# Kernel optimization log

Hardware: AMD Instinct MI355X
Metric: run time of the kernel (lower is better)

## Reference

```python
import jax, jax.numpy as jnp
import numpy as np

N_NODES = 10000
N_EDGES = 160000
N_GRAPHS = 64
IN_DIM, HID, HEADS, OUT_DIM = 128, 64, 8, 10
NEG_SLOPE = 0.2


def setup_inputs() -> dict:
    key = jax.random.key(0)
    ks = jax.random.split(key, 20)
    x = jax.random.normal(ks[0], (N_NODES, IN_DIM), dtype=jnp.float32)
    edge_index = jax.random.randint(ks[1], (2, N_EDGES), 0, N_NODES, dtype=jnp.int64)
    batch = jnp.sort(jax.random.randint(ks[2], (N_NODES,), 0, N_GRAPHS, dtype=jnp.int64))

    def glorot(k, shape):
        fan_in, fan_out = shape[0], shape[-1]
        lim = jnp.sqrt(6.0 / (fan_in + fan_out)).astype(jnp.float32)
        return jax.random.uniform(k, shape, jnp.float32, -lim, lim)

    d0 = HID * HEADS  # 512
    params = {
        # layer 0: IN_DIM -> HID x HEADS, concat
        'W0': glorot(ks[3], (IN_DIM, HEADS * HID)),
        'asrc0': glorot(ks[4], (HEADS, HID)), 'adst0': glorot(ks[5], (HEADS, HID)),
        'b0': jnp.zeros((HEADS * HID,), jnp.float32),
        # layer 1: 512 -> HID x HEADS, concat
        'W1': glorot(ks[6], (d0, HEADS * HID)),
        'asrc1': glorot(ks[7], (HEADS, HID)), 'adst1': glorot(ks[8], (HEADS, HID)),
        'b1': jnp.zeros((HEADS * HID,), jnp.float32),
        # layer 2: 512 -> HID, heads=1
        'W2': glorot(ks[9], (d0, HID)),
        'asrc2': glorot(ks[10], (1, HID)), 'adst2': glorot(ks[11], (1, HID)),
        'b2': jnp.zeros((HID,), jnp.float32),
        # classifier: 2*HID -> HID -> OUT_DIM
        'cW1': glorot(ks[12], (2 * HID, HID)), 'cb1': jnp.zeros((HID,), jnp.float32),
        'cW2': glorot(ks[13], (HID, OUT_DIM)), 'cb2': jnp.zeros((OUT_DIM,), jnp.float32),
    }
    return {'x': x, 'edge_index': edge_index, 'batch': batch, **params}


def gat_conv(h_in, src, dst, W, a_src, a_dst, b, heads, ch):
    # PyG GATConv (concat=True, negative_slope=0.2), dropout inactive (eval).
    N = h_in.shape[0]
    h = (h_in @ W).reshape(N, heads, ch)                       # [N,H,C]
    a_s = jnp.sum(h * a_src[None], axis=-1)                    # [N,H]
    a_d = jnp.sum(h * a_dst[None], axis=-1)                    # [N,H]
    e = jax.nn.leaky_relu(a_s[src] + a_d[dst], NEG_SLOPE)      # [E,H]
    # per-destination segment softmax (stable)
    m = jax.ops.segment_max(e, dst, num_segments=N)            # [N,H]
    ex = jnp.exp(e - m[dst])
    s = jax.ops.segment_sum(ex, dst, num_segments=N)
    alpha = ex / (s[dst] + 1e-16)                              # [E,H]
    out = jax.ops.segment_sum(h[src] * alpha[:, :, None], dst, num_segments=N)
    return out.reshape(N, heads * ch) + b


def _forward(x, src, dst, batch,
             W0, asrc0, adst0, b0, W1, asrc1, adst1, b1,
             W2, asrc2, adst2, b2, cW1, cb1, cW2, cb2):
    h = gat_conv(x, src, dst, W0, asrc0, adst0, b0, HEADS, HID)
    h = jax.nn.relu(h)
    h = gat_conv(h, src, dst, W1, asrc1, adst1, b1, HEADS, HID)
    h = jax.nn.relu(h)
    h = gat_conv(h, src, dst, W2, asrc2, adst2, b2, 1, HID)    # [N,HID]
    # global mean + max pool over graphs
    sums = jax.ops.segment_sum(h, batch, num_segments=N_GRAPHS)
    cnt = jax.ops.segment_sum(jnp.ones((h.shape[0], 1), h.dtype), batch, num_segments=N_GRAPHS)
    mean = sums / jnp.maximum(cnt, 1.0)
    mx = jax.ops.segment_max(h, batch, num_segments=N_GRAPHS)
    g = jnp.concatenate([mean, mx], axis=1)                    # [G, 2*HID]
    g = jax.nn.relu(g @ cW1 + cb1)
    return g @ cW2 + cb2                                       # [G, OUT_DIM]


def reference(x, edge_index, batch,
              W0, asrc0, adst0, b0, W1, asrc1, adst1, b1,
              W2, asrc2, adst2, b2, cW1, cb1, cW2, cb2):
    # PyG GATConv adds self-loops by default
    loops = jnp.arange(x.shape[0], dtype=edge_index.dtype)
    src = jnp.concatenate([edge_index[0], loops])
    dst = jnp.concatenate([edge_index[1], loops])
    return _forward(x, src, dst, batch,
                    W0, asrc0, adst0, b0, W1, asrc1, adst1, b1,
                    W2, asrc2, adst2, b2, cW1, cb1, cW2, cb2)
```

## Files before the change

kernel.cpp:

```cpp
#include <hip/hip_runtime.h>
#include <hip/hip_bf16.h>
#include <math.h>

#define NN 10000
#define EIN 160000
#define ETOT 170000
#define NG 64
#define INDIM 128
#define HID 64
#define HEADS 8
#define D0 512
#define OUTD 10

using bfrag = __attribute__((ext_vector_type(8))) short;
using ffrag = __attribute__((ext_vector_type(4))) float;

__device__ inline float bf2f(unsigned short u) { return __uint_as_float(((unsigned)u) << 16); }
__device__ inline unsigned short f2bf(float f) {
    __hip_bfloat16 b = __float2bfloat16(f);
    return *reinterpret_cast<unsigned short*>(&b);
}

__device__ void transpose_tile(const float* __restrict__ src, __hip_bfloat16* __restrict__ dst,
                               int R, int C, int bx, int by) {
    __shared__ float tile[32][33];
    int cb = bx * 32, rb = by * 32;
    int tx = threadIdx.x & 31, ty = threadIdx.x >> 5;
#pragma unroll
    for (int i = 0; i < 32; i += 8) {
        int r = rb + ty + i, c = cb + tx;
        tile[ty + i][tx] = (r < R && c < C) ? src[(size_t)r * C + c] : 0.f;
    }
    __syncthreads();
#pragma unroll
    for (int i = 0; i < 32; i += 8) {
        int c = cb + ty + i, r = rb + tx;
        if (c < C && r < R) dst[(size_t)c * R + r] = __float2bfloat16(tile[tx][ty + i]);
    }
}

__global__ __launch_bounds__(256) void prep_kernel(const float* __restrict__ x,
                                                   const float* __restrict__ W0,
                                                   const float* __restrict__ W1,
                                                   const float* __restrict__ W2,
                                                   __hip_bfloat16* __restrict__ xb,
                                                   __hip_bfloat16* __restrict__ W0T,
                                                   __hip_bfloat16* __restrict__ W1T,
                                                   __hip_bfloat16* __restrict__ W2T,
                                                   int* __restrict__ cnt) {
    int bid = blockIdx.x;
    if (bid < 5000) {
        int i = bid * 256 + threadIdx.x;
        xb[i] = __float2bfloat16(x[i]);
    } else if (bid < 5064) {
        int lb = bid - 5000;
        transpose_tile(W0, W0T, INDIM, D0, lb & 15, lb >> 4);
    } else if (bid < 5320) {
        int lb = bid - 5064;
        transpose_tile(W1, W1T, D0, D0, lb & 15, lb >> 4);
    } else if (bid < 5352) {
        int lb = bid - 5320;
        transpose_tile(W2, W2T, D0, 64, lb & 1, lb >> 1);
    } else {
        int i = (bid - 5352) * 256 + threadIdx.x;
        if (i < NN) cnt[i] = 0;
    }
}

__global__ void count_kernel(const int* __restrict__ ei, int* __restrict__ cnt) {
    int i = blockIdx.x * 256 + threadIdx.x;
    if (i >= ETOT) return;
    int dst = (i < EIN) ? ei[EIN + i] : (i - EIN);
    atomicAdd(&cnt[dst], 1);
}

__global__ __launch_bounds__(1024) void scan_kernel(const int* __restrict__ cnt,
                                                    int* __restrict__ row_ptr,
                                                    int* __restrict__ cursor) {
    __shared__ int ssum[1024];
    int t = threadIdx.x;
    const int PER = 10;
    int base = t * PER;
    int loc[PER];
    int s = 0;
#pragma unroll
    for (int i = 0; i < PER; i++) {
        int v = (base + i < NN) ? cnt[base + i] : 0;
        loc[i] = s; s += v;
    }
    ssum[t] = s;
    __syncthreads();
    for (int off = 1; off < 1024; off <<= 1) {
        int v = (t >= off) ? ssum[t - off] : 0;
        __syncthreads();
        ssum[t] += v;
        __syncthreads();
    }
    int bs = (t > 0) ? ssum[t - 1] : 0;
#pragma unroll
    for (int i = 0; i < PER; i++) {
        if (base + i < NN) { int v = bs + loc[i]; row_ptr[base + i] = v; cursor[base + i] = v; }
    }
    if (t == 0) row_ptr[NN] = ssum[1023];
}

__global__ void scatter_kernel(const int* __restrict__ ei, int* __restrict__ cursor,
                               int* __restrict__ col_src) {
    int i = blockIdx.x * 256 + threadIdx.x;
    if (i >= ETOT) return;
    int src, dst;
    if (i < EIN) { src = ei[i]; dst = ei[EIN + i]; }
    else { src = i - EIN; dst = src; }
    int pos = atomicAdd(&cursor[dst], 1);
    col_src[pos] = src;
}

#define GBM 128
#define GBN 128
#define GBK 32
#define LPAD 8

__global__ __launch_bounds__(256) void gemm_attn(const __hip_bfloat16* __restrict__ A,
                                                 const __hip_bfloat16* __restrict__ BT,
                                                 float* __restrict__ C,
                                                 __hip_bfloat16* __restrict__ Cb,
                                                 const float* __restrict__ asrc,
                                                 const float* __restrict__ adst,
                                                 float* __restrict__ a_s,
                                                 float* __restrict__ a_d,
                                                 int H, int M, int N, int K) {
    __shared__ __align__(16) short As[GBM][GBK + LPAD];
    __shared__ __align__(16) short Bs[GBN][GBK + LPAD];
    int tid = threadIdx.x;
    int wid = tid >> 6, lane = tid & 63;
    int wr = wid >> 1, wc = wid & 1;
    int brow = blockIdx.y * GBM, bcol = blockIdx.x * GBN;

    ffrag acc[4][4] = {};

    int srow = tid >> 2;
    int skq  = (tid & 3) * 8;

    int kq = (lane >> 4) * 8;
    int ra = lane & 15;

    for (int k0 = 0; k0 < K; k0 += GBK) {
#pragma unroll
        for (int p = 0; p < 2; ++p) {
            int r = srow + p * 64;
            int gr = brow + r;
            bfrag va = {0,0,0,0,0,0,0,0};
            if (gr < M) va = *(const bfrag*)(A + (size_t)gr * K + k0 + skq);
            *(bfrag*)&As[r][skq] = va;
            int gc = bcol + r;
            bfrag vb = {0,0,0,0,0,0,0,0};
            if (gc < N) vb = *(const bfrag*)(BT + (size_t)gc * K + k0 + skq);
            *(bfrag*)&Bs[r][skq] = vb;
        }
        __syncthreads();
        bfrag af[4], bf[4];
#pragma unroll
        for (int m = 0; m < 4; ++m) af[m] = *(const bfrag*)&As[wr * 64 + m * 16 + ra][kq];
#pragma unroll
        for (int n = 0; n < 4; ++n) bf[n] = *(const bfrag*)&Bs[wc * 64 + n * 16 + ra][kq];
#pragma unroll
        for (int m = 0; m < 4; ++m)
#pragma unroll
            for (int n = 0; n < 4; ++n)
                acc[m][n] = __builtin_amdgcn_mfma_f32_16x16x32_bf16(af[m], bf[n], acc[m][n], 0, 0, 0);
        __syncthreads();
    }

    int cr = (lane >> 4) * 4;
    int cc = lane & 15;

#pragma unroll
    for (int m = 0; m < 4; ++m) {
#pragma unroll
        for (int n = 0; n < 4; ++n) {
#pragma unroll
            for (int r = 0; r < 4; ++r) {
                int grow = brow + wr * 64 + m * 16 + cr + r;
                int gcol = bcol + wc * 64 + n * 16 + cc;
                if (grow < M && gcol < N) {
                    float v = acc[m][n][r];
                    if (C)  C[(size_t)grow * N + gcol] = v;
                    if (Cb) Cb[(size_t)grow * N + gcol] = __float2bfloat16(v);
                }
            }
        }
    }

    int head = (bcol >> 6) + wc;
    if (head < H) {
        float asl[4], adl[4];
        int cbase = head * 64;
#pragma unroll
        for (int n = 0; n < 4; ++n) {
            asl[n] = asrc[cbase + n * 16 + cc];
            adl[n] = adst[cbase + n * 16 + cc];
        }
#pragma unroll
        for (int m = 0; m < 4; ++m) {
#pragma unroll
            for (int r = 0; r < 4; ++r) {
                float ps = 0.f, pd = 0.f;
#pragma unroll
                for (int n = 0; n < 4; ++n) {
                    float av = acc[m][n][r];
                    ps += av * asl[n];
                    pd += av * adl[n];
                }
#pragma unroll
                for (int o = 1; o < 16; o <<= 1) {
                    ps += __shfl_xor(ps, o);
                    pd += __shfl_xor(pd, o);
                }
                if (cc == 0) {
                    int row = brow + wr * 64 + m * 16 + cr + r;
                    if (row < M) {
                        a_s[(size_t)row * H + head] = ps;
                        a_d[(size_t)row * H + head] = pd;
                    }
                }
            }
        }
    }
}

__global__ __launch_bounds__(256) void gat_agg8(const __hip_bfloat16* __restrict__ h,
                                                const float* __restrict__ a_s,
                                                const float* __restrict__ a_d,
                                                const int* __restrict__ row_ptr,
                                                const int* __restrict__ col_src,
                                                const float* __restrict__ bias,
                                                __hip_bfloat16* __restrict__ out)
{
    int n = blockIdx.x;
    int tid = threadIdx.x;
    int hh = tid >> 5;
    int c0 = tid * 2;
    int r0 = row_ptr[n], r1 = row_ptr[n + 1];

    __shared__ float ad_sh[8];
    __shared__ float al_sh[32][8];
    __shared__ int   src_sh[32];
    if (tid < 8) ad_sh[tid] = a_d[n * 8 + tid];

    float acc0 = 0.f, acc1 = 0.f, ss = 0.f;
    const unsigned short* hu = (const unsigned short*)h;

    for (int kb = r0; kb < r1; kb += 32) {
        __syncthreads();
        {
            int eb = tid >> 3, h8 = tid & 7;
            int k = kb + eb;
            int kc = (k < r1) ? k : r1 - 1;
            int s = col_src[kc];
            if (h8 == 0) src_sh[eb] = s;
            float e = a_s[s * 8 + h8] + ad_sh[h8];
            e = e > 0.f ? e : 0.2f * e;
            float al = __expf(e);
            al_sh[eb][h8] = (k < r1) ? al : 0.f;
        }
        __syncthreads();
        int nb = (r1 - kb < 32) ? (r1 - kb) : 32;
        for (int j = 0; j < nb; j += 8) {
            int s[8]; float al[8]; unsigned v[8];
#pragma unroll
            for (int i = 0; i < 8; ++i) s[i] = src_sh[j + i];
#pragma unroll
            for (int i = 0; i < 8; ++i) al[i] = al_sh[j + i][hh];
#pragma unroll
            for (int i = 0; i < 8; ++i) v[i] = *(const unsigned*)(hu + (size_t)s[i] * 512 + c0);
#pragma unroll
            for (int i = 0; i < 8; ++i) {
                acc0 += al[i] * bf2f((unsigned short)(v[i] & 0xffff));
                acc1 += al[i] * bf2f((unsigned short)(v[i] >> 16));
                ss += al[i];
            }
        }
    }
    float inv = 1.f / (ss + 1e-16f);
    float2 bv = *(const float2*)(bias + c0);
    float o0 = fmaxf(acc0 * inv + bv.x, 0.f);
    float o1 = fmaxf(acc1 * inv + bv.y, 0.f);
    unsigned pk = (unsigned)f2bf(o0) | ((unsigned)f2bf(o1) << 16);
    *(unsigned*)((unsigned short*)out + (size_t)n * 512 + c0) = pk;
}

__global__ __launch_bounds__(256) void gat_agg1(const float* __restrict__ h,
                                                const float* __restrict__ a_s,
                                                const float* __restrict__ a_d,
                                                const int* __restrict__ row_ptr,
                                                const int* __restrict__ col_src,
                                                const float* __restrict__ bias,
                                                float* __restrict__ out) {
    int n = blockIdx.x * 4 + (threadIdx.x >> 6);
    int lane = threadIdx.x & 63;
    if (n >= NN) return;
    int r0 = row_ptr[n], r1 = row_ptr[n + 1];
    float ad = a_d[n];
    float acc = 0.f, ssum = 0.f;
    for (int k = r0; k < r1; k += 8) {
        int kk[8]; int s[8]; float av[8]; float v[8];
#pragma unroll
        for (int i = 0; i < 8; ++i) kk[i] = (k + i < r1) ? k + i : r1 - 1;
#pragma unroll
        for (int i = 0; i < 8; ++i) s[i] = col_src[kk[i]];
#pragma unroll
        for (int i = 0; i < 8; ++i) av[i] = a_s[s[i]];
#pragma unroll
        for (int i = 0; i < 8; ++i) v[i] = h[(size_t)s[i] * 64 + lane];
#pragma unroll
        for (int i = 0; i < 8; ++i) {
            float e = av[i] + ad;
            e = e > 0.f ? e : 0.2f * e;
            float al = __expf(e);
            al = (k + i < r1) ? al : 0.f;
            acc += al * v[i];
            ssum += al;
        }
    }
    out[(size_t)n * 64 + lane] = acc / (ssum + 1e-16f) + bias[lane];
}

__global__ __launch_bounds__(256) void pool_classify(const float* __restrict__ h,
                                                     const int* __restrict__ batch,
                                                     const float* __restrict__ cW1, const float* __restrict__ cb1,
                                                     const float* __restrict__ cW2, const float* __restrict__ cb2,
                                                     float* __restrict__ out) {
    int g = blockIdx.x;
    int tid = threadIdx.x;
    int lane = tid & 63, w = tid >> 6;

    int lo = 0, hi = NN;
    while (lo < hi) { int mid = (lo + hi) >> 1; if (batch[mid] < g) lo = mid + 1; else hi = mid; }
    int s = lo;
    lo = s; hi = NN;
    while (lo < hi) { int mid = (lo + hi) >> 1; if (batch[mid] < g + 1) lo = mid + 1; else hi = mid; }
    int e = lo;

    float sum = 0.f, mx = -1e30f;
    for (int n = s + w; n < e; n += 4) {
        float v = h[(size_t)n * 64 + lane];
        sum += v; mx = fmaxf(mx, v);
    }
    __shared__ float ssum[4][64], smax[4][64];
    __shared__ float gv[128], c1[64];
    ssum[w][lane] = sum; smax[w][lane] = mx;
    __syncthreads();
    if (tid < 64) {
        float s4 = ssum[0][tid] + ssum[1][tid] + ssum[2][tid] + ssum[3][tid];
        float m4 = fmaxf(fmaxf(smax[0][tid], smax[1][tid]), fmaxf(smax[2][tid], smax[3][tid]));
        int cntv = e - s;
        float c = (float)(cntv > 1 ? cntv : 1);
        gv[tid] = s4 / c;
        gv[64 + tid] = m4;
    }
    __syncthreads();
    if (tid < 64) {
        float acc = cb1[tid];
        for (int k = 0; k < 128; k++) acc += gv[k] * cW1[k * 64 + tid];
        c1[tid] = fmaxf(acc, 0.f);
    }
    __syncthreads();
    if (tid < OUTD) {
        float o = cb2[tid];
        for (int k = 0; k < 64; k++) o += c1[k] * cW2[k * OUTD + tid];
        out[g * OUTD + tid] = o;
    }
}

extern "C" void kernel_launch(void* const* d_in, const int* in_sizes, int n_in,
                              void* d_out, int out_size, void* d_ws, size_t ws_size,
                              hipStream_t stream) {
    const float* x     = (const float*)d_in[0];
    const int*   ei    = (const int*)d_in[1];
    const int*   batch = (const int*)d_in[2];
    const float* W0    = (const float*)d_in[3];
    const float* asrc0 = (const float*)d_in[4];
    const float* adst0 = (const float*)d_in[5];
    const float* b0    = (const float*)d_in[6];
    const float* W1    = (const float*)d_in[7];
    const float* asrc1 = (const float*)d_in[8];
    const float* adst1 = (const float*)d_in[9];
    const float* b1    = (const float*)d_in[10];
    const float* W2    = (const float*)d_in[11];
    const float* asrc2 = (const float*)d_in[12];
    const float* adst2 = (const float*)d_in[13];
    const float* b2    = (const float*)d_in[14];
    const float* cW1   = (const float*)d_in[15];
    const float* cb1   = (const float*)d_in[16];
    const float* cW2   = (const float*)d_in[17];
    const float* cb2   = (const float*)d_in[18];
    float* out = (float*)d_out;

    char* ws = (char*)d_ws;
    size_t off = 0;
    auto alloc = [&](size_t bytes) { void* p = ws + off; off += (bytes + 255) & ~(size_t)255; return p; };
    __hip_bfloat16* bufAb = (__hip_bfloat16*)alloc((size_t)NN * D0 * 2);
    __hip_bfloat16* bufBb = (__hip_bfloat16*)alloc((size_t)NN * D0 * 2);
    float* bufC  = (float*)alloc((size_t)NN * 64 * 4);
    float* bufD  = (float*)alloc((size_t)NN * 64 * 4);
    __hip_bfloat16* xb   = (__hip_bfloat16*)alloc((size_t)NN * INDIM * 2);
    __hip_bfloat16* W0T  = (__hip_bfloat16*)alloc((size_t)D0 * INDIM * 2);
    __hip_bfloat16* W1T  = (__hip_bfloat16*)alloc((size_t)D0 * D0 * 2);
    __hip_bfloat16* W2T  = (__hip_bfloat16*)alloc((size_t)64 * D0 * 2);
    float* a_s     = (float*)alloc((size_t)NN * HEADS * 4);
    float* a_d     = (float*)alloc((size_t)NN * HEADS * 4);
    int*   cnt     = (int*)alloc((size_t)NN * 4);
    int*   row_ptr = (int*)alloc((size_t)(NN + 1) * 4);
    int*   cursor  = (int*)alloc((size_t)NN * 4);
    int*   col_src = (int*)alloc((size_t)(ETOT + 8) * 4);
    (void)ws_size; (void)n_in; (void)in_sizes; (void)out_size;

    prep_kernel<<<5392, 256, 0, stream>>>(x, W0, W1, W2, xb, W0T, W1T, W2T, cnt);

    count_kernel<<<(ETOT + 255) / 256, 256, 0, stream>>>(ei, cnt);
    scan_kernel<<<1, 1024, 0, stream>>>(cnt, row_ptr, cursor);
    scatter_kernel<<<(ETOT + 255) / 256, 256, 0, stream>>>(ei, cursor, col_src);

    dim3 gg8(D0 / GBN, (NN + GBM - 1) / GBM);
    dim3 gg1(1, (NN + GBM - 1) / GBM);

    gemm_attn<<<gg8, 256, 0, stream>>>(xb, W0T, nullptr, bufAb, asrc0, adst0, a_s, a_d, HEADS, NN, D0, INDIM);
    gat_agg8<<<NN, 256, 0, stream>>>(bufAb, a_s, a_d, row_ptr, col_src, b0, bufBb);

    gemm_attn<<<gg8, 256, 0, stream>>>(bufBb, W1T, nullptr, bufAb, asrc1, adst1, a_s, a_d, HEADS, NN, D0, D0);
    gat_agg8<<<NN, 256, 0, stream>>>(bufAb, a_s, a_d, row_ptr, col_src, b1, bufBb);

    gemm_attn<<<gg1, 256, 0, stream>>>(bufBb, W2T, bufC, nullptr, asrc2, adst2, a_s, a_d, 1, NN, 64, D0);
    gat_agg1<<<(NN + 3) / 4, 256, 0, stream>>>(bufC, a_s, a_d, row_ptr, col_src, b2, bufD);

    pool_classify<<<NG, 256, 0, stream>>>(bufD, batch, cW1, cb1, cW2, cb2, out);
}
```

Before: 185.9 us.

## Aggregate multi-head GAT with one wavefront per node and 16-byte gathers

Rewrites the 8-head aggregation kernel so each 64-lane wavefront handles one destination node, with each lane owning 8 contiguous channels loaded as a 16-byte vector. Edge sources and attention weights are computed per lane and broadcast with shuffles instead of staged through shared memory with block barriers. This aims to cut synchronization overhead and the number of narrow gather loads per node. It trades that for fewer edges in flight per node and more registers per lane.

```diff
diff --git a/kernel.cpp b/kernel.cpp
--- a/kernel.cpp
+++ b/kernel.cpp
@@ -14,6 +14,7 @@
 
 using bfrag = __attribute__((ext_vector_type(8))) short;
 using ffrag = __attribute__((ext_vector_type(4))) float;
+using u32x4 = __attribute__((ext_vector_type(4))) unsigned int;
 
 __device__ inline float bf2f(unsigned short u) { return __uint_as_float(((unsigned)u) << 16); }
 __device__ inline unsigned short f2bf(float f) {
@@ -236,57 +237,56 @@
                                                 const float* __restrict__ bias,
                                                 __hip_bfloat16* __restrict__ out)
 {
-    int n = blockIdx.x;
-    int tid = threadIdx.x;
-    int hh = tid >> 5;
-    int c0 = tid * 2;
+    int n = blockIdx.x * 4 + (threadIdx.x >> 6);
+    int lane = threadIdx.x & 63;
     int r0 = row_ptr[n], r1 = row_ptr[n + 1];
 
-    __shared__ float ad_sh[8];
-    __shared__ float al_sh[32][8];
-    __shared__ int   src_sh[32];
-    if (tid < 8) ad_sh[tid] = a_d[n * 8 + tid];
-
-    float acc0 = 0.f, acc1 = 0.f, ss = 0.f;
+    int head_c = lane & 7;
+    int hme = lane >> 3;
+    float ad_c = a_d[n * 8 + head_c];
+
+    float acc[8] = {};
+    float ss = 0.f;
     const unsigned short* hu = (const unsigned short*)h;
 
-    for (int kb = r0; kb < r1; kb += 32) {
-        __syncthreads();
-        {
-            int eb = tid >> 3, h8 = tid & 7;
-            int k = kb + eb;
-            int kc = (k < r1) ? k : r1 - 1;
-            int s = col_src[kc];
-            if (h8 == 0) src_sh[eb] = s;
-            float e = a_s[s * 8 + h8] + ad_sh[h8];
-            e = e > 0.f ? e : 0.2f * e;
-            float al = __expf(e);
-            al_sh[eb][h8] = (k < r1) ? al : 0.f;
-        }
-        __syncthreads();
-        int nb = (r1 - kb < 32) ? (r1 - kb) : 32;
-        for (int j = 0; j < nb; j += 8) {
-            int s[8]; float al[8]; unsigned v[8];
-#pragma unroll
-            for (int i = 0; i < 8; ++i) s[i] = src_sh[j + i];
-#pragma unroll
-            for (int i = 0; i < 8; ++i) al[i] = al_sh[j + i][hh];
-#pragma unroll
-            for (int i = 0; i < 8; ++i) v[i] = *(const unsigned*)(hu + (size_t)s[i] * 512 + c0);
-#pragma unroll
-            for (int i = 0; i < 8; ++i) {
-                acc0 += al[i] * bf2f((unsigned short)(v[i] & 0xffff));
-                acc1 += al[i] * bf2f((unsigned short)(v[i] >> 16));
-                ss += al[i];
+    for (int kb = r0; kb < r1; kb += 8) {
+        int k = kb + (lane >> 3);
+        int kc = (k < r1) ? k : r1 - 1;
+        int s_l = col_src[kc];
+        float e = a_s[s_l * 8 + head_c] + ad_c;
+        e = e > 0.f ? e : 0.2f * e;
+        float al_l = (k < r1) ? __expf(e) : 0.f;
+#pragma unroll
+        for (int j = 0; j < 8; ++j) {
+            int   sj = __shfl(s_l, j * 8);
+            float aj = __shfl(al_l, j * 8 + hme);
+            u32x4 v = *(const u32x4*)(hu + (size_t)sj * 512 + (lane << 3));
+#pragma unroll
+            for (int q = 0; q < 4; ++q) {
+                acc[2 * q]     += aj * bf2f((unsigned short)(v[q] & 0xffff));
+                acc[2 * q + 1] += aj * bf2f((unsigned short)(v[q] >> 16));
             }
-        }
-    }
+            ss += aj;
+        }
+    }
+
     float inv = 1.f / (ss + 1e-16f);
-    float2 bv = *(const float2*)(bias + c0);
-    float o0 = fmaxf(acc0 * inv + bv.x, 0.f);
-    float o1 = fmaxf(acc1 * inv + bv.y, 0.f);
-    unsigned pk = (unsigned)f2bf(o0) | ((unsigned)f2bf(o1) << 16);
-    *(unsigned*)((unsigned short*)out + (size_t)n * 512 + c0) = pk;
+    float4 b0v = *(const float4*)(bias + lane * 8);
+    float4 b1v = *(const float4*)(bias + lane * 8 + 4);
+    float ov[8];
+    ov[0] = fmaxf(acc[0] * inv + b0v.x, 0.f);
+    ov[1] = fmaxf(acc[1] * inv + b0v.y, 0.f);
+    ov[2] = fmaxf(acc[2] * inv + b0v.z, 0.f);
+    ov[3] = fmaxf(acc[3] * inv + b0v.w, 0.f);
+    ov[4] = fmaxf(acc[4] * inv + b1v.x, 0.f);
+    ov[5] = fmaxf(acc[5] * inv + b1v.y, 0.f);
+    ov[6] = fmaxf(acc[6] * inv + b1v.z, 0.f);
+    ov[7] = fmaxf(acc[7] * inv + b1v.w, 0.f);
+    u32x4 pk;
+#pragma unroll
+    for (int q = 0; q < 4; ++q)
+        pk[q] = (unsigned)f2bf(ov[2 * q]) | ((unsigned)f2bf(ov[2 * q + 1]) << 16);
+    *(u32x4*)((unsigned short*)out + (size_t)n * 512 + (lane << 3)) = pk;
 }
 
 __global__ __launch_bounds__(256) void gat_agg1(const float* __restrict__ h,
@@ -425,10 +425,10 @@
     dim3 gg1(1, (NN + GBM - 1) / GBM);
 
     gemm_attn<<<gg8, 256, 0, stream>>>(xb, W0T, nullptr, bufAb, asrc0, adst0, a_s, a_d, HEADS, NN, D0, INDIM);
-    gat_agg8<<<NN, 256, 0, stream>>>(bufAb, a_s, a_d, row_ptr, col_src, b0, bufBb);
+    gat_agg8<<<2500, 256, 0, stream>>>(bufAb, a_s, a_d, row_ptr, col_src, b0, bufBb);
 
     gemm_attn<<<gg8, 256, 0, stream>>>(bufBb, W1T, nullptr, bufAb, asrc1, adst1, a_s, a_d, HEADS, NN, D0, D0);
-    gat_agg8<<<NN, 256, 0, stream>>>(bufAb, a_s, a_d, row_ptr, col_src, b1, bufBb);
+    gat_agg8<<<2500, 256, 0, stream>>>(bufAb, a_s, a_d, row_ptr, col_src, b1, bufBb);
 
     gemm_attn<<<gg1, 256, 0, stream>>>(bufBb, W2T, bufC, nullptr, asrc2, adst2, a_s, a_d, 1, NN, 64, D0);
     gat_agg1<<<(NN + 3) / 4, 256, 0, stream>>>(bufC, a_s, a_d, row_ptr, col_src, b2, bufD);
```

Result: no change. 183.1 us (-1.5%).
